# Optimization experiments

Hardware: AMD Instinct MI355X
Metric: run time of the kernel (lower is better)

## Reference

```python
import jax, jax.numpy as jnp
import numpy as np
from jax import lax

B = 2          # graphs per batch
N_PER = 8192   # points per graph
K = 64         # max_num_neighbors in radius()
RATIO1, R1 = 0.5, 0.2
RATIO2, R2 = 0.25, 0.4


def _init(key, shape):
    return 0.1 * jax.random.normal(key, shape, jnp.float32)


def setup_inputs() -> dict:
    key = jax.random.key(0)
    ks = jax.random.split(key, 16)
    inp = {}
    inp["pos"] = jax.random.uniform(ks[0], (B * N_PER, 3), jnp.float32)
    inp["batch"] = jnp.repeat(jnp.arange(B, dtype=jnp.int32), N_PER)
    i = 1
    for name, dims in [("sa1", [(3, 64), (64, 64), (64, 128)]),
                       ("sa2", [(131, 128), (128, 128), (128, 256)])]:
        for j, (a, b) in enumerate(dims, 1):
            inp[f"{name}_W{j}"] = _init(ks[i], (a, b)); i += 1
            inp[f"{name}_b{j}"] = jnp.zeros((b,), jnp.float32)
    for name, (a, b) in [("lin1", (256, 256)), ("lin2", (256, 128)), ("lin3", (128, 1))]:
        inp[f"{name}_W"] = _init(ks[i], (a, b)); i += 1
        inp[f"{name}_b"] = jnp.zeros((b,), jnp.float32)
    return inp


def _fps(pts, S):
    # farthest point sampling; pts [n,3] -> idx [S] (deterministic start at 0)
    n = pts.shape[0]
    d0 = jnp.full((n,), jnp.inf, pts.dtype)
    def body(carry, _):
        d, last = carry
        d = jnp.minimum(d, jnp.sum((pts - pts[last]) ** 2, axis=-1))
        nxt = jnp.argmax(d).astype(jnp.int32)
        return (d, nxt), last
    _, idx = lax.scan(body, (d0, jnp.int32(0)), None, length=S)
    return idx


def _mlp(h, Ws, bs):
    h = jax.nn.relu(h @ Ws[0] + bs[0])
    h = jax.nn.relu(h @ Ws[1] + bs[1])
    return h @ Ws[2] + bs[2]


def _sa(x, pos, ratio, r, Ws, bs):
    # PointNet++ set abstraction: FPS -> radius neighbors (<=K) -> edge MLP -> max
    # pos [B,n,3]; x [B,n,C] or None
    n = pos.shape[1]
    S = int(n * ratio)
    idx = jax.vmap(lambda p: _fps(p, S))(pos)                       # [B,S]
    q = jnp.take_along_axis(pos, idx[..., None], axis=1)             # [B,S,3]
    d2 = jnp.sum((q[:, :, None, :] - pos[:, None, :, :]) ** 2, -1)   # [B,S,n]
    d2 = jnp.where(d2 <= r * r, d2, jnp.inf)
    negd, nbr = lax.top_k(-d2, K)                                    # [B,S,K]
    valid = jnp.isfinite(negd)                                       # in-radius mask
    gat = jax.vmap(lambda a, i: a[i])                                # per-graph gather
    rel = gat(pos, nbr) - q[:, :, None, :]                           # [B,S,K,3]
    feat = rel if x is None else jnp.concatenate([gat(x, nbr), rel], axis=-1)
    h = _mlp(feat, Ws, bs)                                           # [B,S,K,C]
    h = jnp.where(valid[..., None], h, -jnp.inf)
    return jnp.max(h, axis=2), q                                     # scatter-max aggr


def reference(pos, batch,
              sa1_W1, sa1_b1, sa1_W2, sa1_b2, sa1_W3, sa1_b3,
              sa2_W1, sa2_b1, sa2_W2, sa2_b2, sa2_W3, sa2_b3,
              lin1_W, lin1_b, lin2_W, lin2_b, lin3_W, lin3_b):
    p = pos.reshape(B, N_PER, 3)  # batch ids are sorted, equal-sized graphs
    x1, p1 = _sa(None, p, RATIO1, R1,
                 (sa1_W1, sa1_W2, sa1_W3), (sa1_b1, sa1_b2, sa1_b3))
    x2, _ = _sa(x1, p1, RATIO2, R2,
                (sa2_W1, sa2_W2, sa2_W3), (sa2_b1, sa2_b2, sa2_b3))
    h = jax.nn.relu(x2 @ lin1_W + lin1_b)
    h = jax.nn.relu(h @ lin2_W + lin2_b)
    h = jax.nn.sigmoid(h @ lin3_W + lin3_b)
    return h.reshape(-1, 1)  # [B * N_PER * RATIO1 * RATIO2, 1]
```

## Files before the change

### kernel.cpp

```cpp
#include <hip/hip_runtime.h>
#include <math.h>

#define NEG_INF (-__builtin_inff())
#define POS_INF (__builtin_inff())

__device__ __forceinline__ int imax_i(int a, int b) { return a > b ? a : b; }

template<int CTRL, int RMASK>
__device__ __forceinline__ int dpp_imax_step(int y) {
  const int t = __builtin_amdgcn_update_dpp(y, y, CTRL, RMASK, 0xf, false);
  return imax_i(y, t);
}

template<int N, int PPT, int S, int NT>
__global__ __launch_bounds__(NT) void fpsp_kernel(const float* __restrict__ pos,
                                                  float* __restrict__ q_out)
{
  constexpr int CELLS = 4096;
  constexpr int CPT = CELLS / NT;
  static_assert(N == NT * PPT, "chunking");
  static_assert(S <= CELLS, "winner list fits in hist");

  const int b = blockIdx.x;
  const int t = threadIdx.x;
  pos += (size_t)b * N * 3;
  q_out += (size_t)b * S * 3;

  __shared__ float sxyz[3 * N];
  __shared__ int sorder[N];
  __shared__ int hist[CELLS];
  __shared__ int scanbuf[NT];
  __shared__ unsigned long long slot[4];

  int* const swin = hist;

  for (int i = t; i < CELLS; i += NT) hist[i] = 0;
  if (t < 4) slot[t] = 0;
  __syncthreads();
  for (int i = t; i < N; i += NT) {
    const float x = pos[3*i+0], y = pos[3*i+1], z = pos[3*i+2];
    sxyz[3*i+0] = x; sxyz[3*i+1] = y; sxyz[3*i+2] = z;
    int cx = (int)(x * 16.f); cx = cx < 0 ? 0 : (cx > 15 ? 15 : cx);
    int cy = (int)(y * 16.f); cy = cy < 0 ? 0 : (cy > 15 ? 15 : cy);
    int cz = (int)(z * 16.f); cz = cz < 0 ? 0 : (cz > 15 ? 15 : cz);
    int m = 0;
#pragma unroll
    for (int k = 0; k < 4; ++k)
      m |= (((cx >> k) & 1) << (3*k+2)) | (((cy >> k) & 1) << (3*k+1)) | (((cz >> k) & 1) << (3*k));
    atomicAdd(&hist[m], 1);
  }
  __syncthreads();
  int loc[CPT]; int run = 0;
#pragma unroll
  for (int j = 0; j < CPT; ++j) { loc[j] = run; run += hist[t*CPT + j]; }
  scanbuf[t] = run;
  __syncthreads();
  for (int off = 1; off < NT; off <<= 1) {
    const int o = (t >= off) ? scanbuf[t - off] : 0;
    __syncthreads();
    scanbuf[t] += o;
    __syncthreads();
  }
  const int base = scanbuf[t] - run;
#pragma unroll
  for (int j = 0; j < CPT; ++j) hist[t*CPT + j] = base + loc[j];
  __syncthreads();
  for (int i = t; i < N; i += NT) {
    const float x = sxyz[3*i+0], y = sxyz[3*i+1], z = sxyz[3*i+2];
    int cx = (int)(x * 16.f); cx = cx < 0 ? 0 : (cx > 15 ? 15 : cx);
    int cy = (int)(y * 16.f); cy = cy < 0 ? 0 : (cy > 15 ? 15 : cy);
    int cz = (int)(z * 16.f); cz = cz < 0 ? 0 : (cz > 15 ? 15 : cz);
    int m = 0;
#pragma unroll
    for (int k = 0; k < 4; ++k)
      m |= (((cx >> k) & 1) << (3*k+2)) | (((cy >> k) & 1) << (3*k+1)) | (((cz >> k) & 1) << (3*k));
    const int sl = atomicAdd(&hist[m], 1);
    sorder[sl] = i;
  }
  __syncthreads();
  float px[PPT], py[PPT], pz[PPT], d[PPT];
  int og[PPT];
  float bxmin = POS_INF, bxmax = NEG_INF, bymin = POS_INF, bymax = NEG_INF,
        bzmin = POS_INF, bzmax = NEG_INF;
#pragma unroll
  for (int j = 0; j < PPT; ++j) {
    const int o = sorder[t*PPT + j];
    og[j] = o;
    const float x = sxyz[3*o+0], y = sxyz[3*o+1], z = sxyz[3*o+2];
    px[j] = x; py[j] = y; pz[j] = z;
    bxmin = fminf(bxmin, x); bxmax = fmaxf(bxmax, x);
    bymin = fminf(bymin, y); bymax = fmaxf(bymax, y);
    bzmin = fminf(bzmin, z); bzmax = fmaxf(bzmax, z);
    d[j] = POS_INF;
  }
  __syncthreads();

  const int lane = t & 63;

  float cval = POS_INF;
  int corig = 0x7fffffff;
  int wmvb = 0;
  int wwo = 0x7fffffff;

  int worig = 0;
  int p = 0;

  for (int it = 0; it < S; ++it) {
    if (t == 0) swin[it] = worig;
    const float lx = sxyz[3*worig+0], ly = sxyz[3*worig+1], lz = sxyz[3*worig+2];

    const float ddx = fmaxf(0.f, fmaxf(bxmin - lx, lx - bxmax));
    const float ddy = fmaxf(0.f, fmaxf(bymin - ly, ly - bymax));
    const float ddz = fmaxf(0.f, fmaxf(bzmin - lz, lz - bzmax));
    const float mind2 = ddx*ddx + ddy*ddy + ddz*ddz;
    const bool rec = !(mind2 * 0.99999f >= cval);

    if (rec) {
      float bv = -1.f; int bo = 0x7fffffff;
#pragma unroll
      for (int j = 0; j < PPT; ++j) {
        const float dx = __fsub_rn(px[j], lx);
        const float dy = __fsub_rn(py[j], ly);
        const float dz = __fsub_rn(pz[j], lz);
        const float nd = __fadd_rn(__fadd_rn(__fmul_rn(dx, dx), __fmul_rn(dy, dy)),
                                   __fmul_rn(dz, dz));
        const float dn = __builtin_fminf(d[j], nd);
        d[j] = dn;
        if (dn > bv || (dn == bv && og[j] < bo)) { bv = dn; bo = og[j]; }
      }
      cval = bv; corig = bo;
    }

    if (__ballot(rec) != 0ULL) {
      const int x = __float_as_int(cval);
      int y = x;
      y = dpp_imax_step<0x111, 0xf>(y);
      y = dpp_imax_step<0x112, 0xf>(y);
      y = dpp_imax_step<0x114, 0xf>(y);
      y = dpp_imax_step<0x118, 0xf>(y);
      y = dpp_imax_step<0x142, 0xa>(y);
      y = dpp_imax_step<0x143, 0xc>(y);
      wmvb = __builtin_amdgcn_readlane(y, 63);
      unsigned long long tie = __ballot(__float_as_int(cval) == wmvb);
      int wo = 0x7fffffff;
      while (tie) {
        const int l = __builtin_ctzll(tie);
        const int o = __builtin_amdgcn_readlane(corig, l);
        wo = wo < o ? wo : o;
        tie &= tie - 1;
      }
      wwo = wo;
    }

    if (lane == 0) {
      const unsigned long long mykey =
          ((unsigned long long)(unsigned)wmvb << 32) |
          (unsigned)~(unsigned)wwo;
      if (slot[p] < mykey) atomicMax(&slot[p], mykey);
    }
    if (t == 0) slot[(p + 1) & 3] = 0;
    __syncthreads();
    const unsigned long long wm = slot[p];
    worig = (int)(~(unsigned)(wm & 0xffffffffULL));
    p = (p + 1) & 3;
  }

  __syncthreads();
  for (int s = t; s < S; s += NT) {
    const int o = swin[s];
    q_out[3*s+0] = sxyz[3*o+0]; q_out[3*s+1] = sxyz[3*o+1]; q_out[3*s+2] = sxyz[3*o+2];
  }
}

#define KNN_CAP 2048

__global__ __launch_bounds__(256) void knn_kernel(const float* __restrict__ cand,
                                                  const float* __restrict__ qpos,
                                                  int nq_per_graph, int n_cand, float r2,
                                                  int* __restrict__ nbr_out,
                                                  int* __restrict__ cnt_out)
{
  const int qi = blockIdx.x;
  const int t = threadIdx.x;
  const int b = qi / nq_per_graph;
  const float* cb = cand + (size_t)b * n_cand * 3;
  const float qx = qpos[3*qi+0], qy = qpos[3*qi+1], qz = qpos[3*qi+2];

  __shared__ unsigned long long keys[KNN_CAP];
  __shared__ int s_cnt;
  if (t == 0) s_cnt = 0;
  __syncthreads();

  for (int i = t; i < n_cand; i += 256) {
    const float dx = __fsub_rn(cb[3*i+0], qx);
    const float dy = __fsub_rn(cb[3*i+1], qy);
    const float dz = __fsub_rn(cb[3*i+2], qz);
    const float d2 = __fadd_rn(__fadd_rn(__fmul_rn(dx, dx), __fmul_rn(dy, dy)),
                               __fmul_rn(dz, dz));
    if (d2 <= r2) {
      const int p = atomicAdd(&s_cnt, 1);
      if (p < KNN_CAP) keys[p] = ((unsigned long long)__float_as_uint(d2) << 32) | (unsigned)i;
    }
  }
  __syncthreads();
  const int M = min(s_cnt, KNN_CAP);
  const int out_n = min(M, 64);
  if (M > 64) {
    int P = 128; while (P < M) P <<= 1;
    for (int i = M + t; i < P; i += 256) keys[i] = ~0ULL;
    __syncthreads();
    for (int k = 2; k <= P; k <<= 1) {
      for (int j = k >> 1; j > 0; j >>= 1) {
        for (int i = t; i < P; i += 256) {
          const int l = i ^ j;
          if (l > i) {
            const unsigned long long a = keys[i], c = keys[l];
            const bool up = ((i & k) == 0);
            if ((a > c) == up) { keys[i] = c; keys[l] = a; }
          }
        }
        __syncthreads();
      }
    }
  }
  if (t < 64) nbr_out[(size_t)qi*64 + t] = (t < out_n) ? (int)(keys[t] & 0xffffffffu) : -1;
  if (t == 0) cnt_out[qi] = out_n;
}

__global__ __launch_bounds__(256) void mlp1_kernel(const float* __restrict__ pos,
                                                   const float* __restrict__ q1,
                                                   const int* __restrict__ nbr,
                                                   const int* __restrict__ cnt_,
                                                   const float* __restrict__ W1, const float* __restrict__ b1,
                                                   const float* __restrict__ W2, const float* __restrict__ b2,
                                                   const float* __restrict__ W3, const float* __restrict__ b3,
                                                   float* __restrict__ x1)
{
  const int qi = blockIdx.x;
  const int t = threadIdx.x;
  const int bg = qi >> 12;
  const float* cb = pos + (size_t)bg * 8192 * 3;

  __shared__ float sW1[3*64];
  __shared__ float sb1[64];
  __shared__ float sW2[64*64];
  __shared__ float sb2[64];
  __shared__ float sW3[64*128];
  __shared__ float sb3[128];
  __shared__ float featT[3][64];
  __shared__ float h1[64][65];
  __shared__ float h2b[64][65];

  const int cnt = cnt_[qi];
  const float qx = q1[3*qi+0], qy = q1[3*qi+1], qz = q1[3*qi+2];

  if (t < 64) {
    float r0 = 0.f, r1 = 0.f, r2v = 0.f;
    if (t < cnt) {
      const int nb = nbr[(size_t)qi*64 + t];
      r0 = cb[3*nb+0] - qx;
      r1 = cb[3*nb+1] - qy;
      r2v = cb[3*nb+2] - qz;
    }
    featT[0][t] = r0; featT[1][t] = r1; featT[2][t] = r2v;
  }
  for (int i = t; i < 192; i += 256) sW1[i] = W1[i];
  if (t < 64) { sb1[t] = b1[t]; sb2[t] = b2[t]; }
  for (int i = t; i < 4096; i += 256) sW2[i] = W2[i];
  for (int i = t; i < 8192; i += 256) sW3[i] = W3[i];
  if (t < 128) sb3[t] = b3[t];
  __syncthreads();

  const int e = t & 63, cg = t >> 6;
  {
    const int c0 = cg * 16;
    const float a0 = featT[0][e], a1 = featT[1][e], a2 = featT[2][e];
#pragma unroll
    for (int i = 0; i < 16; ++i) {
      float v = sb1[c0+i];
      v = fmaf(a0, sW1[0*64 + c0+i], v);
      v = fmaf(a1, sW1[1*64 + c0+i], v);
      v = fmaf(a2, sW1[2*64 + c0+i], v);
      h1[e][c0+i] = fmaxf(v, 0.f);
    }
  }
  __syncthreads();
  {
    const int c0 = cg * 16;
    float acc[16];
#pragma unroll
    for (int i = 0; i < 16; ++i) acc[i] = sb2[c0+i];
    for (int k = 0; k < 64; ++k) {
      const float a = h1[e][k];
      const float4* wp = reinterpret_cast<const float4*>(&sW2[k*64 + c0]);
#pragma unroll
      for (int i = 0; i < 4; ++i) {
        const float4 w = wp[i];
        acc[4*i+0] = fmaf(a, w.x, acc[4*i+0]);
        acc[4*i+1] = fmaf(a, w.y, acc[4*i+1]);
        acc[4*i+2] = fmaf(a, w.z, acc[4*i+2]);
        acc[4*i+3] = fmaf(a, w.w, acc[4*i+3]);
      }
    }
#pragma unroll
    for (int i = 0; i < 16; ++i) h2b[e][c0+i] = fmaxf(acc[i], 0.f);
  }
  __syncthreads();
  float acc3[32];
  const int c0h = cg * 32;
  {
#pragma unroll
    for (int i = 0; i < 32; ++i) acc3[i] = sb3[c0h+i];
    for (int k = 0; k < 64; ++k) {
      const float a = h2b[e][k];
      const float4* wp = reinterpret_cast<const float4*>(&sW3[k*128 + c0h]);
#pragma unroll
      for (int i = 0; i < 8; ++i) {
        const float4 w = wp[i];
        acc3[4*i+0] = fmaf(a, w.x, acc3[4*i+0]);
        acc3[4*i+1] = fmaf(a, w.y, acc3[4*i+1]);
        acc3[4*i+2] = fmaf(a, w.z, acc3[4*i+2]);
        acc3[4*i+3] = fmaf(a, w.w, acc3[4*i+3]);
      }
    }
  }
  __syncthreads();
  {
    const bool valid = (e < cnt);
#pragma unroll
    for (int i = 0; i < 32; ++i) {
      const float v = valid ? acc3[i] : NEG_INF;
      const int c = c0h + i;
      if (c < 64) h1[e][c] = v; else h2b[e][c-64] = v;
    }
  }
  __syncthreads();
  if (t < 128) {
    float m = NEG_INF;
    if (t < 64) {
      for (int ee = 0; ee < 64; ++ee) m = fmaxf(m, h1[ee][t]);
    } else {
      for (int ee = 0; ee < 64; ++ee) m = fmaxf(m, h2b[ee][t-64]);
    }
    x1[(size_t)qi*128 + t] = m;
  }
}

__global__ __launch_bounds__(256) void mlp2_kernel(const float* __restrict__ q1,
                                                   const float* __restrict__ x1,
                                                   const float* __restrict__ q2,
                                                   const int* __restrict__ nbr,
                                                   const int* __restrict__ cnt_,
                                                   const float* __restrict__ W1, const float* __restrict__ b1,
                                                   const float* __restrict__ W2, const float* __restrict__ b2,
                                                   const float* __restrict__ W3, const float* __restrict__ b3,
                                                   float* __restrict__ x2)
{
  const int qi = blockIdx.x;
  const int t = threadIdx.x;
  const int bg = qi >> 10;
  const float* cb = q1 + (size_t)bg * 4096 * 3;
  const float* xb = x1 + (size_t)bg * 4096 * 128;

  __shared__ float sW[131*128];
  __shared__ float sb[256];
  __shared__ float featT[131][64];
  __shared__ float hbuf[64][129];
  __shared__ int snb[64];

  const int cnt = cnt_[qi];
  const float qx = q2[3*qi+0], qy = q2[3*qi+1], qz = q2[3*qi+2];

  if (t < 64) {
    const int nb = (t < cnt) ? nbr[(size_t)qi*64 + t] : 0;
    snb[t] = nb;
    float r0 = 0.f, r1 = 0.f, r2v = 0.f;
    if (t < cnt) {
      r0 = cb[3*nb+0] - qx;
      r1 = cb[3*nb+1] - qy;
      r2v = cb[3*nb+2] - qz;
    }
    featT[128][t] = r0; featT[129][t] = r1; featT[130][t] = r2v;
  }
  for (int i = t; i < 131*128; i += 256) sW[i] = W1[i];
  if (t < 128) sb[t] = b1[t];
  __syncthreads();
  for (int idx = t; idx < 64*128; idx += 256) {
    const int e = idx >> 7, k = idx & 127;
    featT[k][e] = (e < cnt) ? xb[(size_t)snb[e]*128 + k] : 0.f;
  }
  __syncthreads();

  const int e = t & 63, cg = t >> 6, c0 = cg * 32;
  float acc[32];
  {
#pragma unroll
    for (int i = 0; i < 32; ++i) acc[i] = sb[c0+i];
    for (int k = 0; k < 131; ++k) {
      const float a = featT[k][e];
      const float4* wp = reinterpret_cast<const float4*>(&sW[k*128 + c0]);
#pragma unroll
      for (int i = 0; i < 8; ++i) {
        const float4 w = wp[i];
        acc[4*i+0] = fmaf(a, w.x, acc[4*i+0]);
        acc[4*i+1] = fmaf(a, w.y, acc[4*i+1]);
        acc[4*i+2] = fmaf(a, w.z, acc[4*i+2]);
        acc[4*i+3] = fmaf(a, w.w, acc[4*i+3]);
      }
    }
#pragma unroll
    for (int i = 0; i < 32; ++i) hbuf[e][c0+i] = fmaxf(acc[i], 0.f);
  }
  __syncthreads();
  for (int i = t; i < 128*128; i += 256) sW[i] = W2[i];
  if (t < 128) sb[t] = b2[t];
  __syncthreads();
  {
#pragma unroll
    for (int i = 0; i < 32; ++i) acc[i] = sb[c0+i];
    for (int k = 0; k < 128; ++k) {
      const float a = hbuf[e][k];
      const float4* wp = reinterpret_cast<const float4*>(&sW[k*128 + c0]);
#pragma unroll
      for (int i = 0; i < 8; ++i) {
        const float4 w = wp[i];
        acc[4*i+0] = fmaf(a, w.x, acc[4*i+0]);
        acc[4*i+1] = fmaf(a, w.y, acc[4*i+1]);
        acc[4*i+2] = fmaf(a, w.z, acc[4*i+2]);
        acc[4*i+3] = fmaf(a, w.w, acc[4*i+3]);
      }
    }
  }
  __syncthreads();
#pragma unroll
  for (int i = 0; i < 32; ++i) featT[c0+i][e] = fmaxf(acc[i], 0.f);
  __syncthreads();
  for (int hh = 0; hh < 2; ++hh) {
    for (int i = t; i < 128*128; i += 256) {
      const int k = i >> 7, c = i & 127;
      sW[i] = W3[k*256 + hh*128 + c];
    }
    if (t < 128) sb[t] = b3[hh*128 + t];
    __syncthreads();
#pragma unroll
    for (int i = 0; i < 32; ++i) acc[i] = sb[c0+i];
    for (int k = 0; k < 128; ++k) {
      const float a = featT[k][e];
      const float4* wp = reinterpret_cast<const float4*>(&sW[k*128 + c0]);
#pragma unroll
      for (int i = 0; i < 8; ++i) {
        const float4 w = wp[i];
        acc[4*i+0] = fmaf(a, w.x, acc[4*i+0]);
        acc[4*i+1] = fmaf(a, w.y, acc[4*i+1]);
        acc[4*i+2] = fmaf(a, w.z, acc[4*i+2]);
        acc[4*i+3] = fmaf(a, w.w, acc[4*i+3]);
      }
    }
    const bool valid = (e < cnt);
#pragma unroll
    for (int i = 0; i < 32; ++i) hbuf[e][c0+i] = valid ? acc[i] : NEG_INF;
    __syncthreads();
    if (t < 128) {
      float m = NEG_INF;
      for (int ee = 0; ee < 64; ++ee) m = fmaxf(m, hbuf[ee][t]);
      x2[(size_t)qi*256 + hh*128 + t] = m;
    }
    __syncthreads();
  }
}

__global__ __launch_bounds__(256) void head_kernel(const float* __restrict__ x2,
                                                   const float* __restrict__ W1, const float* __restrict__ b1,
                                                   const float* __restrict__ W2, const float* __restrict__ b2,
                                                   const float* __restrict__ W3, const float* __restrict__ b3,
                                                   float* __restrict__ out)
{
  const int pt = blockIdx.x;
  const int t = threadIdx.x;
  __shared__ float sx[256];
  __shared__ float sh1[256];
  __shared__ float sh2[128];
  __shared__ float red[128];

  sx[t] = x2[(size_t)pt*256 + t];
  __syncthreads();
  float a1 = b1[t];
  for (int k = 0; k < 256; ++k) a1 = fmaf(sx[k], W1[k*256 + t], a1);
  sh1[t] = fmaxf(a1, 0.f);
  __syncthreads();
  if (t < 128) {
    float a2 = b2[t];
    for (int k = 0; k < 256; ++k) a2 = fmaf(sh1[k], W2[k*128 + t], a2);
    sh2[t] = fmaxf(a2, 0.f);
  }
  __syncthreads();
  if (t < 128) red[t] = sh2[t] * W3[t];
  __syncthreads();
  for (int o = 64; o > 0; o >>= 1) {
    if (t < o) red[t] += red[t + o];
    __syncthreads();
  }
  if (t == 0) {
    const float v = red[0] + b3[0];
    out[pt] = 1.f / (1.f + expf(-v));
  }
}

extern "C" void kernel_launch(void* const* d_in, const int* in_sizes, int n_in,
                              void* d_out, int out_size, void* d_ws, size_t ws_size,
                              hipStream_t stream)
{
  (void)in_sizes; (void)n_in; (void)out_size; (void)ws_size;
  const float* pos  = (const float*)d_in[0];
  const float* s1W1 = (const float*)d_in[2];  const float* s1b1 = (const float*)d_in[3];
  const float* s1W2 = (const float*)d_in[4];  const float* s1b2 = (const float*)d_in[5];
  const float* s1W3 = (const float*)d_in[6];  const float* s1b3 = (const float*)d_in[7];
  const float* s2W1 = (const float*)d_in[8];  const float* s2b1 = (const float*)d_in[9];
  const float* s2W2 = (const float*)d_in[10]; const float* s2b2 = (const float*)d_in[11];
  const float* s2W3 = (const float*)d_in[12]; const float* s2b3 = (const float*)d_in[13];
  const float* l1W  = (const float*)d_in[14]; const float* l1b  = (const float*)d_in[15];
  const float* l2W  = (const float*)d_in[16]; const float* l2b  = (const float*)d_in[17];
  const float* l3W  = (const float*)d_in[18]; const float* l3b  = (const float*)d_in[19];
  float* out = (float*)d_out;

  char* w = (char*)d_ws;
  size_t off = 0;
  auto alloc = [&](size_t bytes) -> void* {
    void* p = w + off;
    off += (bytes + 255) & ~(size_t)255;
    return p;
  };
  float* q1   = (float*)alloc((size_t)2*4096*3*4);
  float* q2   = (float*)alloc((size_t)2*1024*3*4);
  float* x1   = (float*)alloc((size_t)8192*128*4);
  float* x2   = (float*)alloc((size_t)2048*256*4);
  int*   nbr1 = (int*)alloc((size_t)8192*64*4);
  int*   cnt1 = (int*)alloc((size_t)8192*4);
  int*   nbr2 = (int*)alloc((size_t)2048*64*4);
  int*   cnt2 = (int*)alloc((size_t)2048*4);

  const float R1SQ = (float)(0.2 * 0.2);
  const float R2SQ = (float)(0.4 * 0.4);

  fpsp_kernel<8192, 8, 4096, 1024><<<dim3(2), dim3(1024), 0, stream>>>(pos, q1);
  knn_kernel<<<dim3(8192), dim3(256), 0, stream>>>(pos, q1, 4096, 8192, R1SQ, nbr1, cnt1);
  mlp1_kernel<<<dim3(8192), dim3(256), 0, stream>>>(pos, q1, nbr1, cnt1,
                                                    s1W1, s1b1, s1W2, s1b2, s1W3, s1b3, x1);
  fpsp_kernel<4096, 4, 1024, 1024><<<dim3(2), dim3(1024), 0, stream>>>(q1, q2);
  knn_kernel<<<dim3(2048), dim3(256), 0, stream>>>(q1, q2, 1024, 4096, R2SQ, nbr2, cnt2);
  mlp2_kernel<<<dim3(2048), dim3(256), 0, stream>>>(q1, x1, q2, nbr2, cnt2,
                                                    s2W1, s2b1, s2W2, s2b2, s2W3, s2b3, x2);
  head_kernel<<<dim3(2048), dim3(256), 0, stream>>>(x2, l1W, l1b, l2W, l2b, l3W, l3b, out);
}
```

Baseline: 5.219 ms.

## Fuse stage-1 FPS with neighbor search and MLP in a producer-consumer persistent kernel

Replaces the separate stage-1 FPS, kNN and MLP launches with one persistent kernel. Two blocks run farthest point sampling and publish sampled centroids in chunks of 256 through a global progress counter. The other 254 blocks spin on that counter and, for each ready centroid, do the radius search, bitonic sort and edge MLP with max pooling. The aim is to hide the serial FPS latency behind the neighbor and MLP work and to drop the nbr1/cnt1 round trip through global memory. The risks are spin-wait deadlock if not all blocks are co-resident, and lower per-block efficiency with 1024-thread consumer blocks.

Result: slower. 9.892 ms (+89.5%).

```diff
diff --git a/kernel.cpp b/kernel.cpp
--- a/kernel.cpp
+++ b/kernel.cpp
@@ -10,6 +10,355 @@
 __device__ __forceinline__ int dpp_imax_step(int y) {
   const int t = __builtin_amdgcn_update_dpp(y, y, CTRL, RMASK, 0xf, false);
   return imax_i(y, t);
+}
+
+struct ProdS {
+  unsigned long long slot[4];
+  float sxyz[3 * 8192];
+  int sorder[8192];
+  int hist[4096];
+  int scanbuf[1024];
+};
+struct ConsS {
+  unsigned long long keys[1024];
+  float sW2[64 * 64];
+  float sW3[64 * 128];
+  float sW1[3 * 64];
+  float sb1[64], sb2[64], sb3[128];
+  float h1[64][65];
+  float h2b[64][65];
+  float featT[3][64];
+  float qxyz[3];
+  int snb[64];
+  int s_cnt;
+};
+constexpr size_t SM1 = sizeof(ProdS) > sizeof(ConsS) ? sizeof(ProdS) : sizeof(ConsS);
+
+__global__ __launch_bounds__(1024, 4)
+void stage1_kernel(const float* __restrict__ pos,
+                   float* __restrict__ q1,
+                   float* __restrict__ x1,
+                   unsigned int* __restrict__ progress,
+                   const float* __restrict__ W1, const float* __restrict__ b1,
+                   const float* __restrict__ W2, const float* __restrict__ b2,
+                   const float* __restrict__ W3, const float* __restrict__ b3)
+{
+  constexpr int N = 8192, PPT = 8, S = 4096, NT = 1024;
+  constexpr int CELLS = 4096, CPT = CELLS / NT;
+  __shared__ __align__(16) char smraw[SM1];
+  const int bid = blockIdx.x;
+  const int t = threadIdx.x;
+
+  if (bid < 2) {
+    ProdS& P = *reinterpret_cast<ProdS*>(smraw);
+    const float* pb = pos + (size_t)bid * N * 3;
+    float* qb = q1 + (size_t)bid * S * 3;
+    int* const swin = P.hist;
+
+    for (int i = t; i < CELLS; i += NT) P.hist[i] = 0;
+    if (t < 4) P.slot[t] = 0;
+    __syncthreads();
+    for (int i = t; i < N; i += NT) {
+      const float x = pb[3*i+0], y = pb[3*i+1], z = pb[3*i+2];
+      P.sxyz[3*i+0] = x; P.sxyz[3*i+1] = y; P.sxyz[3*i+2] = z;
+      int cx = (int)(x * 16.f); cx = cx < 0 ? 0 : (cx > 15 ? 15 : cx);
+      int cy = (int)(y * 16.f); cy = cy < 0 ? 0 : (cy > 15 ? 15 : cy);
+      int cz = (int)(z * 16.f); cz = cz < 0 ? 0 : (cz > 15 ? 15 : cz);
+      int m = 0;
+#pragma unroll
+      for (int k = 0; k < 4; ++k)
+        m |= (((cx >> k) & 1) << (3*k+2)) | (((cy >> k) & 1) << (3*k+1)) | (((cz >> k) & 1) << (3*k));
+      atomicAdd(&P.hist[m], 1);
+    }
+    __syncthreads();
+    int loc[CPT]; int run = 0;
+#pragma unroll
+    for (int j = 0; j < CPT; ++j) { loc[j] = run; run += P.hist[t*CPT + j]; }
+    P.scanbuf[t] = run;
+    __syncthreads();
+    for (int off = 1; off < NT; off <<= 1) {
+      const int o = (t >= off) ? P.scanbuf[t - off] : 0;
+      __syncthreads();
+      P.scanbuf[t] += o;
+      __syncthreads();
+    }
+    const int base = P.scanbuf[t] - run;
+#pragma unroll
+    for (int j = 0; j < CPT; ++j) P.hist[t*CPT + j] = base + loc[j];
+    __syncthreads();
+    for (int i = t; i < N; i += NT) {
+      const float x = P.sxyz[3*i+0], y = P.sxyz[3*i+1], z = P.sxyz[3*i+2];
+      int cx = (int)(x * 16.f); cx = cx < 0 ? 0 : (cx > 15 ? 15 : cx);
+      int cy = (int)(y * 16.f); cy = cy < 0 ? 0 : (cy > 15 ? 15 : cy);
+      int cz = (int)(z * 16.f); cz = cz < 0 ? 0 : (cz > 15 ? 15 : cz);
+      int m = 0;
+#pragma unroll
+      for (int k = 0; k < 4; ++k)
+        m |= (((cx >> k) & 1) << (3*k+2)) | (((cy >> k) & 1) << (3*k+1)) | (((cz >> k) & 1) << (3*k));
+      const int sl = atomicAdd(&P.hist[m], 1);
+      P.sorder[sl] = i;
+    }
+    __syncthreads();
+    float px[PPT], py[PPT], pz[PPT], d[PPT];
+    int og[PPT];
+    float bxmin = POS_INF, bxmax = NEG_INF, bymin = POS_INF, bymax = NEG_INF,
+          bzmin = POS_INF, bzmax = NEG_INF;
+#pragma unroll
+    for (int j = 0; j < PPT; ++j) {
+      const int o = P.sorder[t*PPT + j];
+      og[j] = o;
+      const float x = P.sxyz[3*o+0], y = P.sxyz[3*o+1], z = P.sxyz[3*o+2];
+      px[j] = x; py[j] = y; pz[j] = z;
+      bxmin = fminf(bxmin, x); bxmax = fmaxf(bxmax, x);
+      bymin = fminf(bymin, y); bymax = fmaxf(bymax, y);
+      bzmin = fminf(bzmin, z); bzmax = fmaxf(bzmax, z);
+      d[j] = POS_INF;
+    }
+    __syncthreads();
+
+    const int lane = t & 63;
+    float cval = POS_INF;
+    int corig = 0x7fffffff;
+    int wmvb = 0;
+    int wwo = 0x7fffffff;
+    int worig = 0;
+    int p = 0;
+    int pend = 0;
+
+    for (int it = 0; it < S; ++it) {
+      if (it && (it & 255) == 0) {
+        for (int i = it - 256 + t; i < it; i += NT) {
+          const int o = swin[i];
+          qb[3*i+0] = P.sxyz[3*o+0]; qb[3*i+1] = P.sxyz[3*o+1]; qb[3*i+2] = P.sxyz[3*o+2];
+        }
+        pend = it;
+      }
+      if (t == 0) swin[it] = worig;
+      const float lx = P.sxyz[3*worig+0], ly = P.sxyz[3*worig+1], lz = P.sxyz[3*worig+2];
+
+      const float ddx = fmaxf(0.f, fmaxf(bxmin - lx, lx - bxmax));
+      const float ddy = fmaxf(0.f, fmaxf(bymin - ly, ly - bymax));
+      const float ddz = fmaxf(0.f, fmaxf(bzmin - lz, lz - bzmax));
+      const float mind2 = ddx*ddx + ddy*ddy + ddz*ddz;
+      const bool rec = !(mind2 * 0.99999f >= cval);
+
+      if (rec) {
+        float bv = -1.f; int bo = 0x7fffffff;
+#pragma unroll
+        for (int j = 0; j < PPT; ++j) {
+          const float dx = __fsub_rn(px[j], lx);
+          const float dy = __fsub_rn(py[j], ly);
+          const float dz = __fsub_rn(pz[j], lz);
+          const float nd = __fadd_rn(__fadd_rn(__fmul_rn(dx, dx), __fmul_rn(dy, dy)),
+                                     __fmul_rn(dz, dz));
+          const float dn = __builtin_fminf(d[j], nd);
+          d[j] = dn;
+          if (dn > bv || (dn == bv && og[j] < bo)) { bv = dn; bo = og[j]; }
+        }
+        cval = bv; corig = bo;
+      }
+
+      if (__ballot(rec) != 0ULL) {
+        const int x = __float_as_int(cval);
+        int y = x;
+        y = dpp_imax_step<0x111, 0xf>(y);
+        y = dpp_imax_step<0x112, 0xf>(y);
+        y = dpp_imax_step<0x114, 0xf>(y);
+        y = dpp_imax_step<0x118, 0xf>(y);
+        y = dpp_imax_step<0x142, 0xa>(y);
+        y = dpp_imax_step<0x143, 0xc>(y);
+        wmvb = __builtin_amdgcn_readlane(y, 63);
+        unsigned long long tie = __ballot(__float_as_int(cval) == wmvb);
+        int wo = 0x7fffffff;
+        while (tie) {
+          const int l = __builtin_ctzll(tie);
+          const int o = __builtin_amdgcn_readlane(corig, l);
+          wo = wo < o ? wo : o;
+          tie &= tie - 1;
+        }
+        wwo = wo;
+      }
+
+      if (lane == 0)
+        atomicMax(&P.slot[p], ((unsigned long long)(unsigned)wmvb << 32) |
+                              (unsigned)~(unsigned)wwo);
+      if (t == 0) P.slot[(p + 1) & 3] = 0;
+      __syncthreads();
+      if (pend && t == 0) {
+        __threadfence();
+        __hip_atomic_store(&progress[bid], (unsigned)pend,
+                           __ATOMIC_RELEASE, __HIP_MEMORY_SCOPE_AGENT);
+      }
+      pend = 0;
+      const unsigned long long wm = P.slot[p];
+      worig = (int)(~(unsigned)(wm & 0xffffffffULL));
+      p = (p + 1) & 3;
+    }
+
+    __syncthreads();
+    for (int i = S - 256 + t; i < S; i += NT) {
+      const int o = swin[i];
+      qb[3*i+0] = P.sxyz[3*o+0]; qb[3*i+1] = P.sxyz[3*o+1]; qb[3*i+2] = P.sxyz[3*o+2];
+    }
+    __syncthreads();
+    if (t == 0) {
+      __threadfence();
+      __hip_atomic_store(&progress[bid], (unsigned)S,
+                         __ATOMIC_RELEASE, __HIP_MEMORY_SCOPE_AGENT);
+    }
+    return;
+  }
+
+  ConsS& C = *reinterpret_cast<ConsS*>(smraw);
+  const float R1SQ = (float)(0.2 * 0.2);
+
+  for (int i = t; i < 192; i += 1024) C.sW1[i] = W1[i];
+  if (t < 64) { C.sb1[t] = b1[t]; C.sb2[t] = b2[t]; }
+  for (int i = t; i < 4096; i += 1024) C.sW2[i] = W2[i];
+  for (int i = t; i < 8192; i += 1024) C.sW3[i] = W3[i];
+  if (t < 128) C.sb3[t] = b3[t];
+  __syncthreads();
+
+  const int e = t & 63, cg = t >> 6;
+
+  for (int qi = bid - 2; qi < 8192; qi += 254) {
+    const int g = qi >> 12;
+    const int s = qi & 4095;
+    if (t == 0) {
+      while (__hip_atomic_load(&progress[g], __ATOMIC_ACQUIRE,
+                               __HIP_MEMORY_SCOPE_AGENT) <= (unsigned)s)
+        __builtin_amdgcn_s_sleep(32);
+#pragma unroll
+      for (int c = 0; c < 3; ++c) {
+        const unsigned u = __hip_atomic_load(
+            (const unsigned*)(q1 + (size_t)3*qi + c),
+            __ATOMIC_RELAXED, __HIP_MEMORY_SCOPE_AGENT);
+        C.qxyz[c] = __uint_as_float(u);
+      }
+      C.s_cnt = 0;
+    }
+    __syncthreads();
+    const float qx = C.qxyz[0], qy = C.qxyz[1], qz = C.qxyz[2];
+    const float* cb = pos + (size_t)g * 8192 * 3;
+
+    for (int i = t; i < 8192; i += 1024) {
+      const float dx = __fsub_rn(cb[3*i+0], qx);
+      const float dy = __fsub_rn(cb[3*i+1], qy);
+      const float dz = __fsub_rn(cb[3*i+2], qz);
+      const float d2 = __fadd_rn(__fadd_rn(__fmul_rn(dx, dx), __fmul_rn(dy, dy)),
+                                 __fmul_rn(dz, dz));
+      if (d2 <= R1SQ) {
+        const int pp = atomicAdd(&C.s_cnt, 1);
+        if (pp < 1024)
+          C.keys[pp] = ((unsigned long long)__float_as_uint(d2) << 32) | (unsigned)i;
+      }
+    }
+    __syncthreads();
+    const int M = min(C.s_cnt, 1024);
+    const int cnt = min(M, 64);
+    if (M > 64) {
+      int P2 = 128; while (P2 < M) P2 <<= 1;
+      for (int i = M + t; i < P2; i += 1024) C.keys[i] = ~0ULL;
+      __syncthreads();
+      for (int k = 2; k <= P2; k <<= 1) {
+        for (int j = k >> 1; j > 0; j >>= 1) {
+          if (t < P2) {
+            const int l = t ^ j;
+            if (l > t) {
+              const unsigned long long a = C.keys[t], c = C.keys[l];
+              const bool up = ((t & k) == 0);
+              if ((a > c) == up) { C.keys[t] = c; C.keys[l] = a; }
+            }
+          }
+          __syncthreads();
+        }
+      }
+    }
+    if (t < 64) C.snb[t] = (t < cnt) ? (int)(C.keys[t] & 0xffffffffu) : 0;
+    __syncthreads();
+
+    if (t < 64) {
+      float r0 = 0.f, r1 = 0.f, r2v = 0.f;
+      if (t < cnt) {
+        const int nb = C.snb[t];
+        r0 = cb[3*nb+0] - qx;
+        r1 = cb[3*nb+1] - qy;
+        r2v = cb[3*nb+2] - qz;
+      }
+      C.featT[0][t] = r0; C.featT[1][t] = r1; C.featT[2][t] = r2v;
+    }
+    __syncthreads();
+    {
+      const int c0 = cg * 4;
+      const float a0 = C.featT[0][e], a1 = C.featT[1][e], a2 = C.featT[2][e];
+#pragma unroll
+      for (int i = 0; i < 4; ++i) {
+        float v = C.sb1[c0+i];
+        v = fmaf(a0, C.sW1[0*64 + c0+i], v);
+        v = fmaf(a1, C.sW1[1*64 + c0+i], v);
+        v = fmaf(a2, C.sW1[2*64 + c0+i], v);
+        C.h1[e][c0+i] = fmaxf(v, 0.f);
+      }
+    }
+    __syncthreads();
+    {
+      const int c0 = cg * 4;
+      float acc[4];
+#pragma unroll
+      for (int i = 0; i < 4; ++i) acc[i] = C.sb2[c0+i];
+      for (int k = 0; k < 64; ++k) {
+        const float a = C.h1[e][k];
+        const float4 w = *reinterpret_cast<const float4*>(&C.sW2[k*64 + c0]);
+        acc[0] = fmaf(a, w.x, acc[0]);
+        acc[1] = fmaf(a, w.y, acc[1]);
+        acc[2] = fmaf(a, w.z, acc[2]);
+        acc[3] = fmaf(a, w.w, acc[3]);
+      }
+#pragma unroll
+      for (int i = 0; i < 4; ++i) C.h2b[e][c0+i] = fmaxf(acc[i], 0.f);
+    }
+    __syncthreads();
+    float acc3[8];
+    const int c0h = cg * 8;
+    {
+#pragma unroll
+      for (int i = 0; i < 8; ++i) acc3[i] = C.sb3[c0h+i];
+      for (int k = 0; k < 64; ++k) {
+        const float a = C.h2b[e][k];
+        const float4* wp = reinterpret_cast<const float4*>(&C.sW3[k*128 + c0h]);
+        const float4 w0 = wp[0], w1 = wp[1];
+        acc3[0] = fmaf(a, w0.x, acc3[0]);
+        acc3[1] = fmaf(a, w0.y, acc3[1]);
+        acc3[2] = fmaf(a, w0.z, acc3[2]);
+        acc3[3] = fmaf(a, w0.w, acc3[3]);
+        acc3[4] = fmaf(a, w1.x, acc3[4]);
+        acc3[5] = fmaf(a, w1.y, acc3[5]);
+        acc3[6] = fmaf(a, w1.z, acc3[6]);
+        acc3[7] = fmaf(a, w1.w, acc3[7]);
+      }
+    }
+    __syncthreads();
+    {
+      const bool valid = (e < cnt);
+#pragma unroll
+      for (int i = 0; i < 8; ++i) {
+        const float v = valid ? acc3[i] : NEG_INF;
+        const int c = c0h + i;
+        if (c < 64) C.h1[e][c] = v; else C.h2b[e][c-64] = v;
+      }
+    }
+    __syncthreads();
+    if (t < 128) {
+      float m = NEG_INF;
+      if (t < 64) {
+        for (int ee = 0; ee < 64; ++ee) m = fmaxf(m, C.h1[ee][t]);
+      } else {
+        for (int ee = 0; ee < 64; ++ee) m = fmaxf(m, C.h2b[ee][t-64]);
+      }
+      x1[(size_t)qi*128 + t] = m;
+    }
+    __syncthreads();
+  }
 }
 
 template<int N, int PPT, int S, int NT>
@@ -96,12 +445,10 @@
   __syncthreads();
 
   const int lane = t & 63;
-
   float cval = POS_INF;
   int corig = 0x7fffffff;
   int wmvb = 0;
   int wwo = 0x7fffffff;
-
   int worig = 0;
   int p = 0;
 
@@ -152,12 +499,9 @@
       wwo = wo;
     }
 
-    if (lane == 0) {
-      const unsigned long long mykey =
-          ((unsigned long long)(unsigned)wmvb << 32) |
-          (unsigned)~(unsigned)wwo;
-      if (slot[p] < mykey) atomicMax(&slot[p], mykey);
-    }
+    if (lane == 0)
+      atomicMax(&slot[p], ((unsigned long long)(unsigned)wmvb << 32) |
+                          (unsigned)~(unsigned)wwo);
     if (t == 0) slot[(p + 1) & 3] = 0;
     __syncthreads();
     const unsigned long long wm = slot[p];
@@ -225,125 +569,6 @@
   }
   if (t < 64) nbr_out[(size_t)qi*64 + t] = (t < out_n) ? (int)(keys[t] & 0xffffffffu) : -1;
   if (t == 0) cnt_out[qi] = out_n;
-}
-
-__global__ __launch_bounds__(256) void mlp1_kernel(const float* __restrict__ pos,
-                                                   const float* __restrict__ q1,
-                                                   const int* __restrict__ nbr,
-                                                   const int* __restrict__ cnt_,
-                                                   const float* __restrict__ W1, const float* __restrict__ b1,
-                                                   const float* __restrict__ W2, const float* __restrict__ b2,
-                                                   const float* __restrict__ W3, const float* __restrict__ b3,
-                                                   float* __restrict__ x1)
-{
-  const int qi = blockIdx.x;
-  const int t = threadIdx.x;
-  const int bg = qi >> 12;
-  const float* cb = pos + (size_t)bg * 8192 * 3;
-
-  __shared__ float sW1[3*64];
-  __shared__ float sb1[64];
-  __shared__ float sW2[64*64];
-  __shared__ float sb2[64];
-  __shared__ float sW3[64*128];
-  __shared__ float sb3[128];
-  __shared__ float featT[3][64];
-  __shared__ float h1[64][65];
-  __shared__ float h2b[64][65];
-
-  const int cnt = cnt_[qi];
-  const float qx = q1[3*qi+0], qy = q1[3*qi+1], qz = q1[3*qi+2];
-
-  if (t < 64) {
-    float r0 = 0.f, r1 = 0.f, r2v = 0.f;
-    if (t < cnt) {
-      const int nb = nbr[(size_t)qi*64 + t];
-      r0 = cb[3*nb+0] - qx;
-      r1 = cb[3*nb+1] - qy;
-      r2v = cb[3*nb+2] - qz;
-    }
-    featT[0][t] = r0; featT[1][t] = r1; featT[2][t] = r2v;
-  }
-  for (int i = t; i < 192; i += 256) sW1[i] = W1[i];
-  if (t < 64) { sb1[t] = b1[t]; sb2[t] = b2[t]; }
-  for (int i = t; i < 4096; i += 256) sW2[i] = W2[i];
-  for (int i = t; i < 8192; i += 256) sW3[i] = W3[i];
-  if (t < 128) sb3[t] = b3[t];
-  __syncthreads();
-
-  const int e = t & 63, cg = t >> 6;
-  {
-    const int c0 = cg * 16;
-    const float a0 = featT[0][e], a1 = featT[1][e], a2 = featT[2][e];
-#pragma unroll
-    for (int i = 0; i < 16; ++i) {
-      float v = sb1[c0+i];
-      v = fmaf(a0, sW1[0*64 + c0+i], v);
-      v = fmaf(a1, sW1[1*64 + c0+i], v);
-      v = fmaf(a2, sW1[2*64 + c0+i], v);
-      h1[e][c0+i] = fmaxf(v, 0.f);
-    }
-  }
-  __syncthreads();
-  {
-    const int c0 = cg * 16;
-    float acc[16];
-#pragma unroll
-    for (int i = 0; i < 16; ++i) acc[i] = sb2[c0+i];
-    for (int k = 0; k < 64; ++k) {
-      const float a = h1[e][k];
-      const float4* wp = reinterpret_cast<const float4*>(&sW2[k*64 + c0]);
-#pragma unroll
-      for (int i = 0; i < 4; ++i) {
-        const float4 w = wp[i];
-        acc[4*i+0] = fmaf(a, w.x, acc[4*i+0]);
-        acc[4*i+1] = fmaf(a, w.y, acc[4*i+1]);
-        acc[4*i+2] = fmaf(a, w.z, acc[4*i+2]);
-        acc[4*i+3] = fmaf(a, w.w, acc[4*i+3]);
-      }
-    }
-#pragma unroll
-    for (int i = 0; i < 16; ++i) h2b[e][c0+i] = fmaxf(acc[i], 0.f);
-  }
-  __syncthreads();
-  float acc3[32];
-  const int c0h = cg * 32;
-  {
-#pragma unroll
-    for (int i = 0; i < 32; ++i) acc3[i] = sb3[c0h+i];
-    for (int k = 0; k < 64; ++k) {
-      const float a = h2b[e][k];
-      const float4* wp = reinterpret_cast<const float4*>(&sW3[k*128 + c0h]);
-#pragma unroll
-      for (int i = 0; i < 8; ++i) {
-        const float4 w = wp[i];
-        acc3[4*i+0] = fmaf(a, w.x, acc3[4*i+0]);
-        acc3[4*i+1] = fmaf(a, w.y, acc3[4*i+1]);
-        acc3[4*i+2] = fmaf(a, w.z, acc3[4*i+2]);
-        acc3[4*i+3] = fmaf(a, w.w, acc3[4*i+3]);
-      }
-    }
-  }
-  __syncthreads();
-  {
-    const bool valid = (e < cnt);
-#pragma unroll
-    for (int i = 0; i < 32; ++i) {
-      const float v = valid ? acc3[i] : NEG_INF;
-      const int c = c0h + i;
-      if (c < 64) h1[e][c] = v; else h2b[e][c-64] = v;
-    }
-  }
-  __syncthreads();
-  if (t < 128) {
-    float m = NEG_INF;
-    if (t < 64) {
-      for (int ee = 0; ee < 64; ++ee) m = fmaxf(m, h1[ee][t]);
-    } else {
-      for (int ee = 0; ee < 64; ++ee) m = fmaxf(m, h2b[ee][t-64]);
-    }
-    x1[(size_t)qi*128 + t] = m;
-  }
 }
 
 __global__ __launch_bounds__(256) void mlp2_kernel(const float* __restrict__ q1,
@@ -534,18 +759,16 @@
   float* q2   = (float*)alloc((size_t)2*1024*3*4);
   float* x1   = (float*)alloc((size_t)8192*128*4);
   float* x2   = (float*)alloc((size_t)2048*256*4);
-  int*   nbr1 = (int*)alloc((size_t)8192*64*4);
-  int*   cnt1 = (int*)alloc((size_t)8192*4);
   int*   nbr2 = (int*)alloc((size_t)2048*64*4);
   int*   cnt2 = (int*)alloc((size_t)2048*4);
-
-  const float R1SQ = (float)(0.2 * 0.2);
+  unsigned int* progress = (unsigned int*)alloc(2*sizeof(unsigned int));
+
   const float R2SQ = (float)(0.4 * 0.4);
 
-  fpsp_kernel<8192, 8, 4096, 1024><<<dim3(2), dim3(1024), 0, stream>>>(pos, q1);
-  knn_kernel<<<dim3(8192), dim3(256), 0, stream>>>(pos, q1, 4096, 8192, R1SQ, nbr1, cnt1);
-  mlp1_kernel<<<dim3(8192), dim3(256), 0, stream>>>(pos, q1, nbr1, cnt1,
-                                                    s1W1, s1b1, s1W2, s1b2, s1W3, s1b3, x1);
+  hipMemsetAsync(progress, 0, 2*sizeof(unsigned int), stream);
+
+  stage1_kernel<<<dim3(256), dim3(1024), 0, stream>>>(pos, q1, x1, progress,
+                                                      s1W1, s1b1, s1W2, s1b2, s1W3, s1b3);
   fpsp_kernel<4096, 4, 1024, 1024><<<dim3(2), dim3(1024), 0, stream>>>(q1, q2);
   knn_kernel<<<dim3(2048), dim3(256), 0, stream>>>(q1, q2, 1024, 4096, R2SQ, nbr2, cnt2);
   mlp2_kernel<<<dim3(2048), dim3(256), 0, stream>>>(q1, x1, q2, nbr2, cnt2,
```
